# Performance work log

Measured on AMD Instinct MI355X. Metric: run time of the kernel, lower is better.

## Reference

```python
import jax, jax.numpy as jnp
import numpy as np

SCALE = 0.1  # literal .mul(0.1) in the source, not 1/sqrt(d_k)


def setup_inputs() -> dict:
    key = jax.random.key(0)
    kq, kk, kv = jax.random.split(key, 3)
    B, S, D, Dv = 8, 2048, 1024, 1024
    q = jax.random.normal(kq, (B, S, D), dtype=jnp.float32)
    k = jax.random.normal(kk, (B, D, S), dtype=jnp.float32)  # note [B, D, S]: matmul(q, k) with no transpose
    v = jax.random.normal(kv, (B, S, Dv), dtype=jnp.float32)
    return {"q": q, "k": k, "v": v}


def reference(q, k, v):
    # s = (q @ k) * 0.1 ; a = softmax(s, -1) ; dropout in eval -> identity ; r = a @ v
    s = jnp.einsum('bsd,bdt->bst', q, k) * SCALE  # [B, S, S]
    a = jax.nn.softmax(s, axis=-1)
    r = jnp.einsum('bst,btv->bsv', a, v)          # [B, S, Dv]
    return r
```

## Files before the change

kernel.cpp:

```cpp
#include <hip/hip_runtime.h>
#include <stdint.h>

#define SEQ 2048
#define DHK 1024
#define DHV 1024
#define NB 8

typedef __attribute__((ext_vector_type(8))) short bf16x8;
typedef __attribute__((ext_vector_type(4))) float f32x4;

__device__ __forceinline__ unsigned short f2bf(float f) {
    uint32_t u = __builtin_bit_cast(uint32_t, f);
    u += 0x7fffu + ((u >> 16) & 1u);
    return (unsigned short)(u >> 16);
}

__device__ __forceinline__ void gload_lds16(const unsigned short* g, unsigned short* l) {
    __builtin_amdgcn_global_load_lds(
        (const __attribute__((address_space(1))) void*)g,
        (__attribute__((address_space(3))) void*)l,
        16, 0, 0);
}

__global__ __launch_bounds__(256) void cvt_q(const float* __restrict__ in,
                                             unsigned short* __restrict__ out) {
    size_t i = ((size_t)blockIdx.x * 256 + threadIdx.x) * 8;
    float4 v0 = *(const float4*)(in + i);
    float4 v1 = *(const float4*)(in + i + 4);
    ushort4 o0, o1;
    o0.x = f2bf(v0.x); o0.y = f2bf(v0.y); o0.z = f2bf(v0.z); o0.w = f2bf(v0.w);
    o1.x = f2bf(v1.x); o1.y = f2bf(v1.y); o1.z = f2bf(v1.z); o1.w = f2bf(v1.w);
    *(ushort4*)(out + i) = o0;
    *(ushort4*)(out + i + 4) = o1;
}

__global__ __launch_bounds__(256) void tr_cvt(const float* __restrict__ in,
                                              unsigned short* __restrict__ out,
                                              int R, int C) {
    __shared__ float tile[64][65];
    int b  = blockIdx.z;
    int c0 = blockIdx.x * 64, r0 = blockIdx.y * 64;
    const float* ib = in + (size_t)b * R * C;
    unsigned short* ob = out + (size_t)b * R * C;
    int tr = threadIdx.x >> 4;
    int tc = (threadIdx.x & 15) * 4;
#pragma unroll
    for (int it = 0; it < 4; ++it) {
        int r = tr + it * 16;
        float4 v = *(const float4*)(ib + (size_t)(r0 + r) * C + c0 + tc);
        tile[r][tc + 0] = v.x; tile[r][tc + 1] = v.y;
        tile[r][tc + 2] = v.z; tile[r][tc + 3] = v.w;
    }
    __syncthreads();
#pragma unroll
    for (int it = 0; it < 4; ++it) {
        int c = tr + it * 16;
        ushort4 o;
        o.x = f2bf(tile[tc + 0][c]);
        o.y = f2bf(tile[tc + 1][c]);
        o.z = f2bf(tile[tc + 2][c]);
        o.w = f2bf(tile[tc + 3][c]);
        *(ushort4*)(ob + (size_t)(c0 + c) * R + r0 + tc) = o;
    }
}

template <int MODE>
__global__ __launch_bounds__(256) void attn_gemm(const unsigned short* __restrict__ A,
                                                 const unsigned short* __restrict__ Bt,
                                                 void* __restrict__ Cout,
                                                 float* __restrict__ L) {
    constexpr int K  = (MODE == 0) ? DHK : SEQ;
    constexpr int N  = (MODE == 0) ? SEQ : DHV;
    constexpr int GM = SEQ / 128;
    constexpr int GN = N / 128;
    constexpr int PM = (MODE == 0) ? 8 : 4;
    constexpr int PN = (MODE == 0) ? 8 : 4;
    constexpr int NPM = GM / PM;

    __shared__ unsigned short As[128 * 64];
    __shared__ unsigned short Bs[128 * 64];

    int lid   = blockIdx.x;
    int batch = lid & 7;
    int t     = lid >> 3;
    int pi    = t / (PM * PN);
    int wio   = t % (PM * PN);
    int bm    = (pi % NPM) * PM + (wio % PM);
    int bn    = (pi / NPM) * PN + (wio / PM);

    const int tid  = threadIdx.x;
    const int wv   = tid >> 6;
    const int lane = tid & 63;
    const int wm   = wv & 1, wn = wv >> 1;
    const int m16  = lane & 15, q = lane >> 4;

    const unsigned short* Ab = A + (size_t)batch * SEQ * K;
    const unsigned short* Bb = Bt + (size_t)batch * N * K;

    const int lr8 = lane >> 3;
    const int g   = (lane & 7) ^ lr8;
    size_t gA[4], gB[4];
    unsigned short *lA[4], *lB[4];
#pragma unroll
    for (int c = 0; c < 4; ++c) {
        int rloc = wv * 32 + c * 8 + lr8;
        gA[c] = (size_t)(bm * 128 + rloc) * K + g * 8;
        gB[c] = (size_t)(bn * 128 + rloc) * K + g * 8;
        lA[c] = &As[(wv * 32 + c * 8) * 64];
        lB[c] = &Bs[(wv * 32 + c * 8) * 64];
    }

    f32x4 acc[4][4];
#pragma unroll
    for (int i = 0; i < 4; ++i)
#pragma unroll
        for (int j = 0; j < 4; ++j)
#pragma unroll
            for (int e = 0; e < 4; ++e) acc[i][j][e] = 0.0f;

    const int sw = m16 & 7;

    for (int kk = 0; kk < K; kk += 64) {
#pragma unroll
        for (int c = 0; c < 4; ++c) gload_lds16(Ab + gA[c] + kk, lA[c]);
#pragma unroll
        for (int c = 0; c < 4; ++c) gload_lds16(Bb + gB[c] + kk, lB[c]);
        __syncthreads();
#pragma unroll
        for (int ss = 0; ss < 2; ++ss) {
            bf16x8 af[4], bfv[4];
#pragma unroll
            for (int tt = 0; tt < 4; ++tt) {
                int rl = wm * 64 + tt * 16 + m16;
                af[tt]  = *(const bf16x8*)&As[rl * 64 + ((ss * 4 + q) ^ sw) * 8];
                int rb = wn * 64 + tt * 16 + m16;
                bfv[tt] = *(const bf16x8*)&Bs[rb * 64 + ((ss * 4 + q) ^ sw) * 8];
            }
#pragma unroll
            for (int mt = 0; mt < 4; ++mt)
#pragma unroll
                for (int nt = 0; nt < 4; ++nt)
                    acc[mt][nt] = __builtin_amdgcn_mfma_f32_16x16x32_bf16(
                        af[mt], bfv[nt], acc[mt][nt], 0, 0, 0);
        }
        __syncthreads();
    }

    const int i0 = bm * 128 + wm * 64;
    const int t0 = bn * 128 + wn * 64;
    if (MODE == 0) {
        unsigned short* E = (unsigned short*)Cout + (size_t)batch * SEQ * N;
        float rs[4][4];
#pragma unroll
        for (int mt = 0; mt < 4; ++mt)
#pragma unroll
            for (int e = 0; e < 4; ++e) rs[mt][e] = 0.0f;
#pragma unroll
        for (int mt = 0; mt < 4; ++mt)
#pragma unroll
            for (int nt = 0; nt < 4; ++nt)
#pragma unroll
                for (int e = 0; e < 4; ++e) {
                    float v = __expf(0.1f * acc[mt][nt][e]);
                    int i = i0 + mt * 16 + q * 4 + e;
                    int tt = t0 + nt * 16 + m16;
                    E[(size_t)i * N + tt] = f2bf(v);
                    rs[mt][e] += v;
                }
#pragma unroll
        for (int mt = 0; mt < 4; ++mt)
#pragma unroll
            for (int e = 0; e < 4; ++e) {
                float v = rs[mt][e];
                v += __shfl_xor(v, 1);
                v += __shfl_xor(v, 2);
                v += __shfl_xor(v, 4);
                v += __shfl_xor(v, 8);
                if (m16 == 0) atomicAdd(&L[batch * SEQ + i0 + mt * 16 + q * 4 + e], v);
            }
    } else {
        float* O = (float*)Cout + (size_t)batch * SEQ * N;
#pragma unroll
        for (int mt = 0; mt < 4; ++mt)
#pragma unroll
            for (int e = 0; e < 4; ++e) {
                int i = i0 + mt * 16 + q * 4 + e;
                float inv = 1.0f / L[batch * SEQ + i];
#pragma unroll
                for (int nt = 0; nt < 4; ++nt) {
                    int tt = t0 + nt * 16 + m16;
                    O[(size_t)i * N + tt] = acc[mt][nt][e] * inv;
                }
            }
    }
}

extern "C" void kernel_launch(void* const* d_in, const int* in_sizes, int n_in,
                              void* d_out, int out_size, void* d_ws, size_t ws_size,
                              hipStream_t stream) {
    (void)in_sizes; (void)n_in; (void)out_size; (void)ws_size;
    const float* q = (const float*)d_in[0];
    const float* k = (const float*)d_in[1];
    const float* v = (const float*)d_in[2];

    char* ws = (char*)d_ws;
    unsigned short* Qb = (unsigned short*)(ws);
    unsigned short* Kt = (unsigned short*)(ws + 33554432);
    unsigned short* Vt = (unsigned short*)(ws + 67108864);
    unsigned short* E  = (unsigned short*)(ws + 100663296);
    float* L           = (float*)(ws + 167772160);

    hipMemsetAsync(L, 0, NB * SEQ * sizeof(float), stream);

    cvt_q<<<dim3((NB * SEQ * DHK) / (256 * 8)), dim3(256), 0, stream>>>(q, Qb);
    tr_cvt<<<dim3(SEQ / 64, DHK / 64, NB), dim3(256), 0, stream>>>(k, Kt, DHK, SEQ);
    tr_cvt<<<dim3(DHV / 64, SEQ / 64, NB), dim3(256), 0, stream>>>(v, Vt, SEQ, DHV);

    attn_gemm<0><<<dim3(NB * 16 * 16), dim3(256), 0, stream>>>(Qb, Kt, (void*)E, L);
    attn_gemm<1><<<dim3(NB * 16 * 8), dim3(256), 0, stream>>>(E, Vt, d_out, L);
}
```

Before: 407.6 us.

## Double-buffer LDS tiles in attention GEMMs and widen Q conversion per thread

```diff
diff --git a/kernel.cpp b/kernel.cpp
--- a/kernel.cpp
+++ b/kernel.cpp
@@ -24,14 +24,14 @@
 
 __global__ __launch_bounds__(256) void cvt_q(const float* __restrict__ in,
                                              unsigned short* __restrict__ out) {
-    size_t i = ((size_t)blockIdx.x * 256 + threadIdx.x) * 8;
-    float4 v0 = *(const float4*)(in + i);
-    float4 v1 = *(const float4*)(in + i + 4);
-    ushort4 o0, o1;
-    o0.x = f2bf(v0.x); o0.y = f2bf(v0.y); o0.z = f2bf(v0.z); o0.w = f2bf(v0.w);
-    o1.x = f2bf(v1.x); o1.y = f2bf(v1.y); o1.z = f2bf(v1.z); o1.w = f2bf(v1.w);
-    *(ushort4*)(out + i) = o0;
-    *(ushort4*)(out + i + 4) = o1;
+    size_t i = ((size_t)blockIdx.x * 256 + threadIdx.x) * 16;
+#pragma unroll
+    for (int c = 0; c < 4; ++c) {
+        float4 v = *(const float4*)(in + i + c * 4);
+        ushort4 o;
+        o.x = f2bf(v.x); o.y = f2bf(v.y); o.z = f2bf(v.z); o.w = f2bf(v.w);
+        *(ushort4*)(out + i + c * 4) = o;
+    }
 }
 
 __global__ __launch_bounds__(256) void tr_cvt(const float* __restrict__ in,
@@ -72,13 +72,12 @@
     constexpr int K  = (MODE == 0) ? DHK : SEQ;
     constexpr int N  = (MODE == 0) ? SEQ : DHV;
     constexpr int GM = SEQ / 128;
-    constexpr int GN = N / 128;
     constexpr int PM = (MODE == 0) ? 8 : 4;
     constexpr int PN = (MODE == 0) ? 8 : 4;
     constexpr int NPM = GM / PM;
 
-    __shared__ unsigned short As[128 * 64];
-    __shared__ unsigned short Bs[128 * 64];
+    __shared__ unsigned short As[2][128 * 64];
+    __shared__ unsigned short Bs[2][128 * 64];
 
     int lid   = blockIdx.x;
     int batch = lid & 7;
@@ -100,14 +99,13 @@
     const int lr8 = lane >> 3;
     const int g   = (lane & 7) ^ lr8;
     size_t gA[4], gB[4];
-    unsigned short *lA[4], *lB[4];
+    int lofs[4];
 #pragma unroll
     for (int c = 0; c < 4; ++c) {
         int rloc = wv * 32 + c * 8 + lr8;
         gA[c] = (size_t)(bm * 128 + rloc) * K + g * 8;
         gB[c] = (size_t)(bn * 128 + rloc) * K + g * 8;
-        lA[c] = &As[(wv * 32 + c * 8) * 64];
-        lB[c] = &Bs[(wv * 32 + c * 8) * 64];
+        lofs[c] = (wv * 32 + c * 8) * 64;
     }
 
     f32x4 acc[4][4];
@@ -120,21 +118,30 @@
 
     const int sw = m16 & 7;
 
+#pragma unroll
+    for (int c = 0; c < 4; ++c) gload_lds16(Ab + gA[c], &As[0][lofs[c]]);
+#pragma unroll
+    for (int c = 0; c < 4; ++c) gload_lds16(Bb + gB[c], &Bs[0][lofs[c]]);
+
+    int p = 0;
     for (int kk = 0; kk < K; kk += 64) {
-#pragma unroll
-        for (int c = 0; c < 4; ++c) gload_lds16(Ab + gA[c] + kk, lA[c]);
-#pragma unroll
-        for (int c = 0; c < 4; ++c) gload_lds16(Bb + gB[c] + kk, lB[c]);
         __syncthreads();
+        if (kk + 64 < K) {
+            int np = p ^ 1;
+#pragma unroll
+            for (int c = 0; c < 4; ++c) gload_lds16(Ab + gA[c] + kk + 64, &As[np][lofs[c]]);
+#pragma unroll
+            for (int c = 0; c < 4; ++c) gload_lds16(Bb + gB[c] + kk + 64, &Bs[np][lofs[c]]);
+        }
 #pragma unroll
         for (int ss = 0; ss < 2; ++ss) {
             bf16x8 af[4], bfv[4];
 #pragma unroll
             for (int tt = 0; tt < 4; ++tt) {
                 int rl = wm * 64 + tt * 16 + m16;
-                af[tt]  = *(const bf16x8*)&As[rl * 64 + ((ss * 4 + q) ^ sw) * 8];
+                af[tt]  = *(const bf16x8*)&As[p][rl * 64 + ((ss * 4 + q) ^ sw) * 8];
                 int rb = wn * 64 + tt * 16 + m16;
-                bfv[tt] = *(const bf16x8*)&Bs[rb * 64 + ((ss * 4 + q) ^ sw) * 8];
+                bfv[tt] = *(const bf16x8*)&Bs[p][rb * 64 + ((ss * 4 + q) ^ sw) * 8];
             }
 #pragma unroll
             for (int mt = 0; mt < 4; ++mt)
@@ -143,7 +150,7 @@
                     acc[mt][nt] = __builtin_amdgcn_mfma_f32_16x16x32_bf16(
                         af[mt], bfv[nt], acc[mt][nt], 0, 0, 0);
         }
-        __syncthreads();
+        p ^= 1;
     }
 
     const int i0 = bm * 128 + wm * 64;
@@ -212,7 +219,7 @@
 
     hipMemsetAsync(L, 0, NB * SEQ * sizeof(float), stream);
 
-    cvt_q<<<dim3((NB * SEQ * DHK) / (256 * 8)), dim3(256), 0, stream>>>(q, Qb);
+    cvt_q<<<dim3((NB * SEQ * DHK) / (256 * 16)), dim3(256), 0, stream>>>(q, Qb);
     tr_cvt<<<dim3(SEQ / 64, DHK / 64, NB), dim3(256), 0, stream>>>(k, Kt, DHK, SEQ);
     tr_cvt<<<dim3(DHV / 64, SEQ / 64, NB), dim3(256), 0, stream>>>(v, Vt, SEQ, DHV);
 
```

Result: faster. 390.7 us (-4.2%).
